# Performance work log

Hardware: AMD Instinct MI355X
Metric: run time of the kernel (lower is better)

Reference implementation:

```python
import jax, jax.numpy as jnp
import numpy as np

POOL = 7
IMG_H, IMG_W = 1024, 1024
CANONICAL = 224.0  # canonical box size used in the FPN level assignment


def _crop_and_resize(fm, boxes, ph, pw):
    """TF-style crop_and_resize (extrapolation_value=0).

    fm: [C, H, W] feature map; boxes: [N, 4] normalized (y1, x1, y2, x2).
    Returns [N, C, ph, pw] bilinearly sampled crops.
    """
    C, H, W = fm.shape
    y1, x1, y2, x2 = boxes[:, 0], boxes[:, 1], boxes[:, 2], boxes[:, 3]
    ty = jnp.arange(ph, dtype=boxes.dtype) / (ph - 1)  # [ph] in [0,1]
    tx = jnp.arange(pw, dtype=boxes.dtype) / (pw - 1)
    ys = (y1[:, None] + (y2 - y1)[:, None] * ty) * (H - 1)  # [N, ph] image coords
    xs = (x1[:, None] + (x2 - x1)[:, None] * tx) * (W - 1)  # [N, pw]
    yy = jnp.broadcast_to(ys[:, :, None], (ys.shape[0], ph, pw))  # [N, ph, pw]
    xx = jnp.broadcast_to(xs[:, None, :], (xs.shape[0], ph, pw))
    y0f = jnp.floor(yy)
    x0f = jnp.floor(xx)
    wy = yy - y0f
    wx = xx - x0f
    y0 = jnp.clip(y0f.astype(jnp.int32), 0, H - 1)
    y1i = jnp.clip(y0 + 1, 0, H - 1)
    x0 = jnp.clip(x0f.astype(jnp.int32), 0, W - 1)
    x1i = jnp.clip(x0 + 1, 0, W - 1)

    def g(yi, xi):
        return fm[:, yi, xi]  # [C, N, ph, pw]

    val = (g(y0, x0) * ((1 - wy) * (1 - wx))[None]
           + g(y0, x1i) * ((1 - wy) * wx)[None]
           + g(y1i, x0) * (wy * (1 - wx))[None]
           + g(y1i, x1i) * (wy * wx)[None])
    # extrapolation_value = 0 for samples outside the feature map
    inb = (yy >= 0) & (yy <= H - 1) & (xx >= 0) & (xx <= W - 1)
    val = jnp.where(inb[None], val, 0.0)
    return jnp.transpose(val, (1, 0, 2, 3))  # [N, C, ph, pw]


def setup_inputs() -> dict:
    key = jax.random.key(0)
    k1, k2, k3, k4, k5, k6, k7, k8 = jax.random.split(key, 8)
    N = 1000
    y1 = jax.random.uniform(k1, (N, 1)) * 0.7
    x1 = jax.random.uniform(k2, (N, 1)) * 0.7
    hh = jax.random.uniform(k3, (N, 1)) * 0.28 + 0.02
    ww = jax.random.uniform(k4, (N, 1)) * 0.28 + 0.02
    boxes = jnp.concatenate([y1, x1, y1 + hh, x1 + ww], axis=1)[None]  # [1,N,4]
    C = 256
    p2 = jax.random.normal(k5, (1, C, 256, 256), dtype=jnp.float32)
    p3 = jax.random.normal(k6, (1, C, 128, 128), dtype=jnp.float32)
    p4 = jax.random.normal(k7, (1, C, 64, 64), dtype=jnp.float32)
    p5 = jax.random.normal(k8, (1, C, 32, 32), dtype=jnp.float32)
    return {"boxes": boxes, "p2": p2, "p3": p3, "p4": p4, "p5": p5}


def reference(boxes, p2, p3, p4, p5):
    boxes = boxes[0]  # squeeze batch, [N,4]
    fms = [p2[0], p3[0], p4[0], p5[0]]  # each [C,H,W]
    y1, x1, y2, x2 = boxes[:, 0:1], boxes[:, 1:2], boxes[:, 2:3], boxes[:, 3:4]
    h = y2 - y1
    w = x2 - x1
    image_area = jnp.asarray(float(IMG_H * IMG_W), dtype=boxes.dtype)
    roi_level = 4 + jnp.log2(jnp.sqrt(h * w) / (CANONICAL / jnp.sqrt(image_area)))
    roi_level = jnp.clip(jnp.round(roi_level), 2, 5).astype(jnp.int32)[:, 0]  # [N]
    # Boxes are detached before cropping in the original (level_boxes.detach()).
    crop_boxes = jax.lax.stop_gradient(boxes)
    out = jnp.zeros((boxes.shape[0], fms[0].shape[0], POOL, POOL), dtype=boxes.dtype)
    for i, level in enumerate(range(2, 6)):
        crop = _crop_and_resize(fms[i], crop_boxes, POOL, POOL)
        sel = (roi_level == level)[:, None, None, None]
        out = out + jnp.where(sel, crop, 0.0)
    return out  # [N, C, POOL, POOL], original box order (sort restores order)
```

## Files before the change

kernel.cpp:

```cpp
#include <hip/hip_runtime.h>

#define POOL 7
#define NCH 256
#define OUT_PER_BOX (NCH * POOL * POOL)
#define PARTS 7
#define PART_SZ (OUT_PER_BOX / PARTS)
#define ITERS (PART_SZ / 256)

__global__ __launch_bounds__(256) void roi_align_kernel(
    const float* __restrict__ boxes,
    const float* __restrict__ p2,
    const float* __restrict__ p3,
    const float* __restrict__ p4,
    const float* __restrict__ p5,
    float* __restrict__ out,
    int nbox)
{
    const int n    = blockIdx.x % nbox;
    const int part = blockIdx.x / nbox;
    const int tid  = threadIdx.x;

    __shared__ int   s_y0[POOL], s_y1[POOL], s_xb[POOL], s_xcl[POOL];
    __shared__ float s_wy[POOL], s_wx[POOL], s_vy[POOL], s_vx[POOL];

    const float by1 = boxes[n * 4 + 0];
    const float bx1 = boxes[n * 4 + 1];
    const float by2 = boxes[n * 4 + 2];
    const float bx2 = boxes[n * 4 + 3];
    const float h = by2 - by1;
    const float w = bx2 - bx1;

    const float lvlf = 4.0f + log2f(sqrtf(h * w) / 0.21875f);
    int lvl = (int)rintf(lvlf);
    lvl = lvl < 2 ? 2 : (lvl > 5 ? 5 : lvl);

    const float* fm;
    int H;
    switch (lvl) {
        case 2:  fm = p2; H = 256; break;
        case 3:  fm = p3; H = 128; break;
        case 4:  fm = p4; H = 64;  break;
        default: fm = p5; H = 32;  break;
    }
    const float Hm1 = (float)(H - 1);

    if (tid < POOL) {
        const float t = (float)tid * (1.0f / 6.0f);

        const float yy  = (by1 + h * t) * Hm1;
        const float y0f = floorf(yy);
        int y0 = (int)y0f;
        y0 = min(H - 1, max(0, y0));
        s_y0[tid] = y0;
        s_y1[tid] = min(H - 1, y0 + 1);
        s_wy[tid] = yy - y0f;
        s_vy[tid] = (yy >= 0.0f && yy <= Hm1) ? 1.0f : 0.0f;

        const float xx  = (bx1 + w * t) * Hm1;
        const float x0f = floorf(xx);
        int x0 = (int)x0f;
        x0 = min(H - 1, max(0, x0));
        s_xb[tid]  = min(x0, H - 2);
        s_xcl[tid] = (x0 == H - 1) ? 1 : 0;
        s_wx[tid]  = xx - x0f;
        s_vx[tid]  = (xx >= 0.0f && xx <= Hm1) ? 1.0f : 0.0f;
    }
    __syncthreads();

    const size_t out_base = (size_t)n * OUT_PER_BOX + (size_t)part * PART_SZ;
    const int idx0 = part * PART_SZ + tid;
    const int HW = H * H;

    float2 q0[ITERS], q1[ITERS];
    #pragma unroll
    for (int i = 0; i < ITERS; ++i) {
        const int idx = idx0 + i * 256;
        const int c  = idx / 49;
        const int r  = idx - c * 49;
        const int py = r / 7;
        const int px = r - py * 7;

        const float* fmc = fm + (size_t)c * HW;
        const int xb = s_xb[px];
        q0[i] = *(const float2*)(fmc + s_y0[py] * H + xb);
        q1[i] = *(const float2*)(fmc + s_y1[py] * H + xb);
    }

    #pragma unroll
    for (int i = 0; i < ITERS; ++i) {
        const int idx = idx0 + i * 256;
        const int c  = idx / 49;
        const int r  = idx - c * 49;
        const int py = r / 7;
        const int px = r - py * 7;

        const float wy = s_wy[py], wx = s_wx[px];
        const int   cl = s_xcl[px];

        const float v00 = cl ? q0[i].y : q0[i].x;
        const float v01 = q0[i].y;
        const float v10 = cl ? q1[i].y : q1[i].x;
        const float v11 = q1[i].y;

        const float r0 = v00 + wx * (v01 - v00);
        const float r1 = v10 + wx * (v11 - v10);
        float val = (r0 + wy * (r1 - r0)) * s_vy[py] * s_vx[px];

        out[out_base + (size_t)(i * 256 + tid)] = val;
    }
}

extern "C" void kernel_launch(void* const* d_in, const int* in_sizes, int n_in,
                              void* d_out, int out_size, void* d_ws, size_t ws_size,
                              hipStream_t stream) {
    const float* boxes = (const float*)d_in[0];
    const float* p2    = (const float*)d_in[1];
    const float* p3    = (const float*)d_in[2];
    const float* p4    = (const float*)d_in[3];
    const float* p5    = (const float*)d_in[4];
    float* out         = (float*)d_out;

    const int nbox = in_sizes[0] / 4;
    roi_align_kernel<<<nbox * PARTS, 256, 0, stream>>>(boxes, p2, p3, p4, p5, out, nbox);
}
```

Before: 155.0 us.

## Sort boxes by level and Morton order and map contiguous chunks per XCD

Adds a single-block bitonic sort that orders boxes by pyramid level and then by the Morton code of their centres, writing a permutation into the workspace. The main kernel now remaps block indices so that each of the 8 XCDs handles a contiguous run of sorted boxes, with all 7 parts of a box landing on the same XCD. The aim is better L2 reuse of feature-map rows, since spatially nearby boxes share samples and stay within one XCD's cache. The cost is an extra kernel launch with a serial sort, and output writes become scattered in box order.

New measurement: 184.8 us. +19.2%, slower.

```diff
diff --git a/kernel.cpp b/kernel.cpp
--- a/kernel.cpp
+++ b/kernel.cpp
@@ -6,6 +6,66 @@
 #define PARTS 7
 #define PART_SZ (OUT_PER_BOX / PARTS)
 #define ITERS (PART_SZ / 256)
+#define NXCD 8
+
+__device__ __forceinline__ unsigned part1by1(unsigned x) {
+    x &= 0x0000FFFFu;
+    x = (x | (x << 8)) & 0x00FF00FFu;
+    x = (x | (x << 4)) & 0x0F0F0F0Fu;
+    x = (x | (x << 2)) & 0x33333333u;
+    x = (x | (x << 1)) & 0x55555555u;
+    return x;
+}
+
+__global__ __launch_bounds__(1024) void sort_boxes_kernel(
+    const float* __restrict__ boxes, int* __restrict__ perm, int nbox)
+{
+    __shared__ unsigned s_key[1024];
+    const int i = threadIdx.x;
+
+    unsigned key = 0xFFFFFFFFu;
+    if (i < nbox) {
+        const float y1 = boxes[i * 4 + 0];
+        const float x1 = boxes[i * 4 + 1];
+        const float y2 = boxes[i * 4 + 2];
+        const float x2 = boxes[i * 4 + 3];
+        const float h = y2 - y1;
+        const float w = x2 - x1;
+        const float lvlf = 4.0f + log2f(sqrtf(h * w) * (1.0f / 0.21875f));
+        int lvl = (int)rintf(lvlf);
+        lvl = lvl < 2 ? 2 : (lvl > 5 ? 5 : lvl);
+
+        const float cy = 0.5f * (y1 + y2);
+        const float cx = 0.5f * (x1 + x2);
+        unsigned qy = (unsigned)fminf(511.0f, fmaxf(0.0f, cy * 512.0f));
+        unsigned qx = (unsigned)fminf(511.0f, fmaxf(0.0f, cx * 512.0f));
+        const unsigned morton = (part1by1(qy) << 1) | part1by1(qx);
+
+        key = ((unsigned)(lvl - 2) << 28) | (morton << 10) | (unsigned)i;
+    }
+    s_key[i] = key;
+    __syncthreads();
+
+    for (int k = 2; k <= 1024; k <<= 1) {
+        for (int j = k >> 1; j > 0; j >>= 1) {
+            const int p = i ^ j;
+            if (p > i) {
+                const unsigned a = s_key[i];
+                const unsigned b = s_key[p];
+                const bool up = ((i & k) == 0);
+                if ((a > b) == up) { s_key[i] = b; s_key[p] = a; }
+            }
+            __syncthreads();
+        }
+    }
+
+    if (i < nbox) perm[i] = (int)(s_key[i] & 1023u);
+}
+
+__global__ void identity_perm_kernel(int* __restrict__ perm, int nbox) {
+    const int i = blockIdx.x * blockDim.x + threadIdx.x;
+    if (i < nbox) perm[i] = i;
+}
 
 __global__ __launch_bounds__(256) void roi_align_kernel(
     const float* __restrict__ boxes,
@@ -14,11 +74,17 @@
     const float* __restrict__ p4,
     const float* __restrict__ p5,
     float* __restrict__ out,
-    int nbox)
+    const int* __restrict__ perm,
+    int nbox, int cpx)
 {
-    const int n    = blockIdx.x % nbox;
-    const int part = blockIdx.x / nbox;
-    const int tid  = threadIdx.x;
+    const int c    = blockIdx.x & (NXCD - 1);
+    const int k    = blockIdx.x >> 3;
+    const int l    = k / PARTS;
+    const int part = k - l * PARTS;
+    const int s    = c * cpx + l;
+    if (s >= nbox) return;
+    const int n = perm[s];
+    const int tid = threadIdx.x;
 
     __shared__ int   s_y0[POOL], s_y1[POOL], s_xb[POOL], s_xcl[POOL];
     __shared__ float s_wy[POOL], s_wx[POOL], s_vy[POOL], s_vx[POOL];
@@ -75,12 +141,12 @@
     #pragma unroll
     for (int i = 0; i < ITERS; ++i) {
         const int idx = idx0 + i * 256;
-        const int c  = idx / 49;
-        const int r  = idx - c * 49;
-        const int py = r / 7;
-        const int px = r - py * 7;
-
-        const float* fmc = fm + (size_t)c * HW;
+        const int cch = idx / 49;
+        const int r   = idx - cch * 49;
+        const int py  = r / 7;
+        const int px  = r - py * 7;
+
+        const float* fmc = fm + (size_t)cch * HW;
         const int xb = s_xb[px];
         q0[i] = *(const float2*)(fmc + s_y0[py] * H + xb);
         q1[i] = *(const float2*)(fmc + s_y1[py] * H + xb);
@@ -89,10 +155,10 @@
     #pragma unroll
     for (int i = 0; i < ITERS; ++i) {
         const int idx = idx0 + i * 256;
-        const int c  = idx / 49;
-        const int r  = idx - c * 49;
-        const int py = r / 7;
-        const int px = r - py * 7;
+        const int cch = idx / 49;
+        const int r   = idx - cch * 49;
+        const int py  = r / 7;
+        const int px  = r - py * 7;
 
         const float wy = s_wy[py], wx = s_wx[px];
         const int   cl = s_xcl[px];
@@ -119,7 +185,17 @@
     const float* p4    = (const float*)d_in[3];
     const float* p5    = (const float*)d_in[4];
     float* out         = (float*)d_out;
+    int*   perm        = (int*)d_ws;
 
     const int nbox = in_sizes[0] / 4;
-    roi_align_kernel<<<nbox * PARTS, 256, 0, stream>>>(boxes, p2, p3, p4, p5, out, nbox);
-}
+    const int cpx  = (nbox + NXCD - 1) / NXCD;
+
+    if (nbox <= 1024) {
+        sort_boxes_kernel<<<1, 1024, 0, stream>>>(boxes, perm, nbox);
+    } else {
+        identity_perm_kernel<<<(nbox + 255) / 256, 256, 0, stream>>>(perm, nbox);
+    }
+
+    roi_align_kernel<<<NXCD * cpx * PARTS, 256, 0, stream>>>(
+        boxes, p2, p3, p4, p5, out, perm, nbox, cpx);
+}
```

## Precompute sorted box params and process box groups per block with software pipelining

Applied to the files above, without the earlier changes.

A prep kernel computes each box's sampling parameters once and counting-sorts boxes by FPN level and spatial quadrant, writing them to workspace. The main kernel then has each block handle a slice of channels for a group of 8 spatially-near, same-level boxes, reading params from shared memory and double-buffering gathers so one box's loads overlap the previous box's interpolation. The goal is better cache locality for feature-map gathers, less redundant per-block setup, and more memory-level parallelism. The cost is an extra kernel launch, and outputs are now written in sorted order, scattered across boxes. A fallback to the old kernel is kept for when workspace is too small.

Measured after the change: 165.8 us. 6.9% more time.

```diff
diff --git a/kernel.cpp b/kernel.cpp
--- a/kernel.cpp
+++ b/kernel.cpp
@@ -3,18 +3,212 @@
 #define POOL 7
 #define NCH 256
 #define OUT_PER_BOX (NCH * POOL * POOL)
-#define PARTS 7
-#define PART_SZ (OUT_PER_BOX / PARTS)
-#define ITERS (PART_SZ / 256)
+#define NSLICE 28
+#define SLICE_SZ (OUT_PER_BOX / NSLICE)
+#define G 8
+#define NBINS 64
+#define PWORDS 64
+
+
+__device__ __forceinline__ void box_params(
+    const float* __restrict__ boxes, int i, int* __restrict__ P, int* lvl_out)
+{
+    const float by1 = boxes[i * 4 + 0];
+    const float bx1 = boxes[i * 4 + 1];
+    const float by2 = boxes[i * 4 + 2];
+    const float bx2 = boxes[i * 4 + 3];
+    const float h = by2 - by1;
+    const float w = bx2 - bx1;
+    const float lvlf = 4.0f + log2f(sqrtf(h * w) / 0.21875f);
+    int lvl = (int)rintf(lvlf);
+    lvl = lvl < 2 ? 2 : (lvl > 5 ? 5 : lvl);
+    const int H = 256 >> (lvl - 2);
+    const float Hm1 = (float)(H - 1);
+
+    #pragma unroll
+    for (int t = 0; t < POOL; ++t) {
+        const float tt = (float)t * (1.0f / 6.0f);
+
+        const float yy  = (by1 + h * tt) * Hm1;
+        const float y0f = floorf(yy);
+        int y0 = (int)y0f;
+        y0 = min(H - 1, max(0, y0));
+        P[t]      = y0 * H;
+        P[7 + t]  = min(H - 1, y0 + 1) * H;
+        P[28 + t] = __float_as_int(yy - y0f);
+        P[42 + t] = __float_as_int((yy >= 0.0f && yy <= Hm1) ? 1.0f : 0.0f);
+
+        const float xx  = (bx1 + w * tt) * Hm1;
+        const float x0f = floorf(xx);
+        int x0 = (int)x0f;
+        x0 = min(H - 1, max(0, x0));
+        P[14 + t] = min(x0, H - 2);
+        P[21 + t] = (x0 == H - 1) ? 1 : 0;
+        P[35 + t] = __float_as_int(xx - x0f);
+        P[49 + t] = __float_as_int((xx >= 0.0f && xx <= Hm1) ? 1.0f : 0.0f);
+    }
+    P[56] = lvl - 2;
+    P[57] = H;
+    P[58] = H * H;
+    P[59] = i;
+    *lvl_out = lvl;
+}
+
+__global__ __launch_bounds__(1024) void prep_kernel(
+    const float* __restrict__ boxes, int* __restrict__ params, int nbox)
+{
+    __shared__ int s_cnt[NBINS], s_off[NBINS];
+    const int i = threadIdx.x;
+    if (i < NBINS) s_cnt[i] = 0;
+    __syncthreads();
+
+    int bin = -1;
+    if (i < nbox) {
+        const float y1 = boxes[i * 4 + 0];
+        const float x1 = boxes[i * 4 + 1];
+        const float y2 = boxes[i * 4 + 2];
+        const float x2 = boxes[i * 4 + 3];
+        const float h = y2 - y1;
+        const float w = x2 - x1;
+        const float lvlf = 4.0f + log2f(sqrtf(h * w) * (1.0f / 0.21875f));
+        int lvl = (int)rintf(lvlf);
+        lvl = lvl < 2 ? 2 : (lvl > 5 ? 5 : lvl);
+        const float cy = 0.5f * (y1 + y2);
+        const float cx = 0.5f * (x1 + x2);
+        int qy = (int)(cy * 4.0f); qy = qy < 0 ? 0 : (qy > 3 ? 3 : qy);
+        int qx = (int)(cx * 4.0f); qx = qx < 0 ? 0 : (qx > 3 ? 3 : qx);
+        bin = ((lvl - 2) << 4) | (qy << 2) | qx;
+        atomicAdd(&s_cnt[bin], 1);
+    }
+    __syncthreads();
+    if (i == 0) {
+        int acc = 0;
+        for (int b = 0; b < NBINS; ++b) { s_off[b] = acc; acc += s_cnt[b]; }
+    }
+    __syncthreads();
+    if (i < nbox) {
+        const int pos = atomicAdd(&s_off[bin], 1);
+        int dummy;
+        box_params(boxes, i, params + pos * PWORDS, &dummy);
+    }
+}
+
+__global__ void prep_flat_kernel(
+    const float* __restrict__ boxes, int* __restrict__ params, int nbox)
+{
+    const int i = blockIdx.x * blockDim.x + threadIdx.x;
+    if (i >= nbox) return;
+    int dummy;
+    box_params(boxes, i, params + i * PWORDS, &dummy);
+}
+
+#define ISSUE(kk, Q00, Q01, Q10, Q11) do {                                   \
+    const int* P = sp[(kk)];                                                 \
+    const int lv = __builtin_amdgcn_readfirstlane(P[56]);                    \
+    const int HW = __builtin_amdgcn_readfirstlane(P[58]);                    \
+    const float* fm = lv == 0 ? p2 : lv == 1 ? p3 : lv == 2 ? p4 : p5;       \
+    { const int a = c0 * HW + P[14 + px0];                                   \
+      Q00 = *(const float2*)(fm + a + P[py0]);                               \
+      Q01 = *(const float2*)(fm + a + P[7 + py0]); }                         \
+    if (has1) {                                                              \
+      const int a = c1 * HW + P[14 + px1];                                   \
+      Q10 = *(const float2*)(fm + a + P[py1]);                               \
+      Q11 = *(const float2*)(fm + a + P[7 + py1]); }                         \
+} while (0)
+
+#define FINISH(kk, Q00, Q01, Q10, Q11) do {                                  \
+    const int* P = sp[(kk)];                                                 \
+    const int n = __builtin_amdgcn_readfirstlane(P[59]);                     \
+    const size_t ob = (size_t)n * OUT_PER_BOX + s * SLICE_SZ + tid;          \
+    {                                                                        \
+        const float wy = __int_as_float(P[28 + py0]);                        \
+        const float wx = __int_as_float(P[35 + px0]);                        \
+        const float vv = __int_as_float(P[42 + py0]) *                       \
+                         __int_as_float(P[49 + px0]);                        \
+        const int   cl = P[21 + px0];                                        \
+        const float v00 = cl ? Q00.y : Q00.x;                                \
+        const float v01 = Q00.y;                                             \
+        const float v10 = cl ? Q01.y : Q01.x;                                \
+        const float v11 = Q01.y;                                             \
+        const float r0v = v00 + wx * (v01 - v00);                            \
+        const float r1v = v10 + wx * (v11 - v10);                            \
+        out[ob] = (r0v + wy * (r1v - r0v)) * vv;                             \
+    }                                                                        \
+    if (has1) {                                                              \
+        const float wy = __int_as_float(P[28 + py1]);                        \
+        const float wx = __int_as_float(P[35 + px1]);                        \
+        const float vv = __int_as_float(P[42 + py1]) *                       \
+                         __int_as_float(P[49 + px1]);                        \
+        const int   cl = P[21 + px1];                                        \
+        const float v00 = cl ? Q10.y : Q10.x;                                \
+        const float v01 = Q10.y;                                             \
+        const float v10 = cl ? Q11.y : Q11.x;                                \
+        const float v11 = Q11.y;                                             \
+        const float r0v = v00 + wx * (v01 - v00);                            \
+        const float r1v = v10 + wx * (v11 - v10);                            \
+        out[ob + 256] = (r0v + wy * (r1v - r0v)) * vv;                       \
+    }                                                                        \
+} while (0)
 
 __global__ __launch_bounds__(256) void roi_align_kernel(
-    const float* __restrict__ boxes,
     const float* __restrict__ p2,
     const float* __restrict__ p3,
     const float* __restrict__ p4,
     const float* __restrict__ p5,
     float* __restrict__ out,
+    const int* __restrict__ params,
     int nbox)
+{
+    const int s   = blockIdx.x % NSLICE;
+    const int g   = blockIdx.x / NSLICE;
+    const int tid = threadIdx.x;
+    const int base = g * G;
+    const int cnt  = min(G, nbox - base);
+
+    __shared__ int sp[G][PWORDS];
+    {
+        const int total = cnt * PWORDS;
+        for (int j = tid; j < G * PWORDS; j += 256)
+            sp[0][j] = (j < total) ? params[base * PWORDS + j] : 0;
+    }
+    __syncthreads();
+
+    const int idx0 = s * SLICE_SZ + tid;
+    const int c0  = idx0 / 49;
+    const int r0  = idx0 - c0 * 49;
+    const int py0 = r0 / 7;
+    const int px0 = r0 - py0 * 7;
+    const bool has1 = (tid < SLICE_SZ - 256);
+    const int idx1 = idx0 + 256;
+    const int c1  = idx1 / 49;
+    const int r1  = idx1 - c1 * 49;
+    const int py1 = r1 / 7;
+    const int px1 = r1 - py1 * 7;
+
+    float2 A00 = {0,0}, A01 = {0,0}, A10 = {0,0}, A11 = {0,0};
+    float2 B00 = {0,0}, B01 = {0,0}, B10 = {0,0}, B11 = {0,0};
+
+    ISSUE(0, A00, A01, A10, A11);
+    #pragma unroll
+    for (int k = 0; k < G; k += 2) {
+        if (k >= cnt) break;
+        if (k + 1 < cnt) ISSUE(k + 1, B00, B01, B10, B11);
+        FINISH(k, A00, A01, A10, A11);
+        if (k + 1 >= cnt) break;
+        if (k + 2 < cnt) ISSUE(k + 2, A00, A01, A10, A11);
+        FINISH(k + 1, B00, B01, B10, B11);
+    }
+}
+
+#define PARTS 7
+#define PART_SZ (OUT_PER_BOX / PARTS)
+#define ITERS (PART_SZ / 256)
+
+__global__ __launch_bounds__(256) void roi_align_flat_kernel(
+    const float* __restrict__ boxes,
+    const float* __restrict__ p2, const float* __restrict__ p3,
+    const float* __restrict__ p4, const float* __restrict__ p5,
+    float* __restrict__ out, int nbox)
 {
     const int n    = blockIdx.x % nbox;
     const int part = blockIdx.x / nbox;
@@ -29,7 +223,6 @@
     const float bx2 = boxes[n * 4 + 3];
     const float h = by2 - by1;
     const float w = bx2 - bx1;
-
     const float lvlf = 4.0f + log2f(sqrtf(h * w) / 0.21875f);
     int lvl = (int)rintf(lvlf);
     lvl = lvl < 2 ? 2 : (lvl > 5 ? 5 : lvl);
@@ -46,7 +239,6 @@
 
     if (tid < POOL) {
         const float t = (float)tid * (1.0f / 6.0f);
-
         const float yy  = (by1 + h * t) * Hm1;
         const float y0f = floorf(yy);
         int y0 = (int)y0f;
@@ -55,7 +247,6 @@
         s_y1[tid] = min(H - 1, y0 + 1);
         s_wy[tid] = yy - y0f;
         s_vy[tid] = (yy >= 0.0f && yy <= Hm1) ? 1.0f : 0.0f;
-
         const float xx  = (bx1 + w * t) * Hm1;
         const float x0f = floorf(xx);
         int x0 = (int)x0f;
@@ -79,13 +270,11 @@
         const int r  = idx - c * 49;
         const int py = r / 7;
         const int px = r - py * 7;
-
         const float* fmc = fm + (size_t)c * HW;
         const int xb = s_xb[px];
         q0[i] = *(const float2*)(fmc + s_y0[py] * H + xb);
         q1[i] = *(const float2*)(fmc + s_y1[py] * H + xb);
     }
-
     #pragma unroll
     for (int i = 0; i < ITERS; ++i) {
         const int idx = idx0 + i * 256;
@@ -93,20 +282,15 @@
         const int r  = idx - c * 49;
         const int py = r / 7;
         const int px = r - py * 7;
-
         const float wy = s_wy[py], wx = s_wx[px];
         const int   cl = s_xcl[px];
-
         const float v00 = cl ? q0[i].y : q0[i].x;
         const float v01 = q0[i].y;
         const float v10 = cl ? q1[i].y : q1[i].x;
         const float v11 = q1[i].y;
-
         const float r0 = v00 + wx * (v01 - v00);
         const float r1 = v10 + wx * (v11 - v10);
-        float val = (r0 + wy * (r1 - r0)) * s_vy[py] * s_vx[px];
-
-        out[out_base + (size_t)(i * 256 + tid)] = val;
+        out[out_base + (size_t)(i * 256 + tid)] = (r0 + wy * (r1 - r0)) * s_vy[py] * s_vx[px];
     }
 }
 
@@ -121,5 +305,22 @@
     float* out         = (float*)d_out;
 
     const int nbox = in_sizes[0] / 4;
-    roi_align_kernel<<<nbox * PARTS, 256, 0, stream>>>(boxes, p2, p3, p4, p5, out, nbox);
-}
+    const size_t need = (size_t)nbox * PWORDS * sizeof(int);
+
+    if (ws_size < need) {
+        roi_align_flat_kernel<<<nbox * PARTS, 256, 0, stream>>>(
+            boxes, p2, p3, p4, p5, out, nbox);
+        return;
+    }
+
+    int* params = (int*)d_ws;
+    if (nbox <= 1024) {
+        prep_kernel<<<1, 1024, 0, stream>>>(boxes, params, nbox);
+    } else {
+        prep_flat_kernel<<<(nbox + 255) / 256, 256, 0, stream>>>(boxes, params, nbox);
+    }
+
+    const int ngroups = (nbox + G - 1) / G;
+    roi_align_kernel<<<ngroups * NSLICE, 256, 0, stream>>>(
+        p2, p3, p4, p5, out, params, nbox);
+}
```

## Bin ROIs by level and spatial tile, stage shared feature regions in LDS

Applied to the files above, without the earlier changes.

Adds a prep pass that precomputes per-box sampling parameters and buckets level 3-5 boxes into spatial bins with atomically tracked bounding regions. A main kernel then loads each bin's feature-map window for a few channels into LDS once and serves every box in the bin from it, so overlapping boxes reuse the same data. Level-2 boxes keep the direct-gather path through a compacted list. This costs two extra launches, atomics, a serial per-bin loop over boxes, and writes scattered across boxes, with fallback to global reads when the region exceeds LDS.

New measurement: 201.0 us. +29.7%, slower.

```diff
diff --git a/kernel.cpp b/kernel.cpp
--- a/kernel.cpp
+++ b/kernel.cpp
@@ -6,22 +6,47 @@
 #define PARTS 7
 #define PART_SZ (OUT_PER_BOX / PARTS)
 #define ITERS (PART_SZ / 256)
-
-__global__ __launch_bounds__(256) void roi_align_kernel(
-    const float* __restrict__ boxes,
-    const float* __restrict__ p2,
-    const float* __restrict__ p3,
-    const float* __restrict__ p4,
-    const float* __restrict__ p5,
-    float* __restrict__ out,
-    int nbox)
+#define PWORDS 64
+
+#define QGRID 4
+#define NBIN_L (QGRID * QGRID)
+#define NLVL_BINNED 3
+#define NBINS (NBIN_L * NLVL_BINNED)
+#define L2BIN NBINS
+#define NLISTS (NBINS + 1)
+
+#define C3 2
+#define C4 4
+#define C5 4
+#define NCHUNK3 (NCH / C3)
+#define NCHUNK4 (NCH / C4)
+#define NCHUNK5 (NCH / C5)
+#define NBLK3 (NBIN_L * NCHUNK3)
+#define NBLK4 (NBIN_L * NCHUNK4)
+#define NBLK5 (NBIN_L * NCHUNK5)
+#define NBLK_BINNED (NBLK3 + NBLK4 + NBLK5)
+
+#define REGION_FLOATS 12288
+
+
+__global__ void init_kernel(int* __restrict__ meta) {
+    const int i = threadIdx.x;
+    if (i < NLISTS) {
+        meta[i * 8 + 0] = 0;
+        meta[i * 8 + 1] = 0x7fffffff;
+        meta[i * 8 + 2] = -1;
+        meta[i * 8 + 3] = 0x7fffffff;
+        meta[i * 8 + 4] = -1;
+    }
+}
+
+__global__ __launch_bounds__(256) void prep_kernel(
+    const float* __restrict__ boxes, int* __restrict__ params,
+    int* __restrict__ meta, int* __restrict__ lists, int nbox)
 {
-    const int n    = blockIdx.x % nbox;
-    const int part = blockIdx.x / nbox;
-    const int tid  = threadIdx.x;
-
-    __shared__ int   s_y0[POOL], s_y1[POOL], s_xb[POOL], s_xcl[POOL];
-    __shared__ float s_wy[POOL], s_wx[POOL], s_vy[POOL], s_vx[POOL];
+    const int n = blockIdx.x * 4 + (threadIdx.x >> 6);
+    const int j = threadIdx.x & 63;
+    if (n >= nbox) return;
 
     const float by1 = boxes[n * 4 + 0];
     const float bx1 = boxes[n * 4 + 1];
@@ -29,7 +54,246 @@
     const float bx2 = boxes[n * 4 + 3];
     const float h = by2 - by1;
     const float w = bx2 - bx1;
-
+    const float lvlf = 4.0f + log2f(sqrtf(h * w) / 0.21875f);
+    int lvl = (int)rintf(lvlf);
+    lvl = lvl < 2 ? 2 : (lvl > 5 ? 5 : lvl);
+    const int H = 256 >> (lvl - 2);
+    const float Hm1 = (float)(H - 1);
+
+    const int t = j % 7;
+    const float tt = (float)t * (1.0f / 6.0f);
+
+    const float yy  = (by1 + h * tt) * Hm1;
+    const float y0f = floorf(yy);
+    int y0 = (int)y0f; y0 = min(H - 1, max(0, y0));
+    const int y1c = min(H - 1, y0 + 1);
+
+    const float xx  = (bx1 + w * tt) * Hm1;
+    const float x0f = floorf(xx);
+    int x0 = (int)x0f; x0 = min(H - 1, max(0, x0));
+    const int xb  = min(x0, H - 2);
+    const int xcl = (x0 == H - 1) ? 1 : 0;
+
+    int val;
+    switch (j / 7) {
+        case 0: val = y0;   break;
+        case 1: val = y1c;  break;
+        case 2: val = xb;   break;
+        case 3: val = xcl;  break;
+        case 4: val = __float_as_int(yy - y0f); break;
+        case 5: val = __float_as_int(xx - x0f); break;
+        case 6: val = __float_as_int((yy >= 0.0f && yy <= Hm1) ? 1.0f : 0.0f); break;
+        case 7: val = __float_as_int((xx >= 0.0f && xx <= Hm1) ? 1.0f : 0.0f); break;
+        default: {
+            const int r = j - 56;
+            val = (r == 0) ? (lvl - 2) : (r == 1) ? H : (r == 2) ? H * H
+                : (r == 3) ? n : 0;
+        }
+    }
+    params[n * PWORDS + j] = val;
+
+    if (j == 0) {
+        if (lvl == 2) {
+            const int slot = atomicAdd(&meta[L2BIN * 8 + 0], 1);
+            lists[L2BIN * nbox + slot] = n;
+        } else {
+            const float cy = 0.5f * (by1 + by2);
+            const float cx = 0.5f * (bx1 + bx2);
+            int qy = (int)(cy * 4.0f); qy = qy < 0 ? 0 : (qy > 3 ? 3 : qy);
+            int qx = (int)(cx * 4.0f); qx = qx < 0 ? 0 : (qx > 3 ? 3 : qx);
+            const int bin = (lvl - 3) * NBIN_L + qy * QGRID + qx;
+            const int slot = atomicAdd(&meta[bin * 8 + 0], 1);
+            lists[bin * nbox + slot] = n;
+            const float yy6 = (by1 + h) * Hm1;
+            int y06 = (int)floorf(yy6); y06 = min(H - 1, max(0, y06));
+            const int y16 = min(H - 1, y06 + 1);
+            const float xx6 = (bx1 + w) * Hm1;
+            int x06 = (int)floorf(xx6); x06 = min(H - 1, max(0, x06));
+            const int xb6 = min(x06, H - 2);
+            atomicMin(&meta[bin * 8 + 1], y0);
+            atomicMax(&meta[bin * 8 + 2], y16);
+            atomicMin(&meta[bin * 8 + 3], xb);
+            atomicMax(&meta[bin * 8 + 4], xb6 + 1);
+        }
+    }
+}
+
+__global__ __launch_bounds__(256) void main_kernel(
+    const float* __restrict__ p2,
+    const float* __restrict__ p3,
+    const float* __restrict__ p4,
+    const float* __restrict__ p5,
+    float* __restrict__ out,
+    const int* __restrict__ params,
+    const int* __restrict__ meta,
+    const int* __restrict__ lists,
+    int nbox)
+{
+    __shared__ float region[REGION_FLOATS];
+    __shared__ int sPm[2 * PWORDS];
+
+    const int bid = blockIdx.x;
+    const int tid = threadIdx.x;
+
+    if (bid >= NBLK_BINNED) {
+        const int bid2 = bid - NBLK_BINNED;
+        const int rank = bid2 / PARTS;
+        const int part = bid2 - rank * PARTS;
+        if (rank >= meta[L2BIN * 8 + 0]) return;
+        const int n = lists[L2BIN * nbox + rank];
+        if (tid < PWORDS) sPm[tid] = params[n * PWORDS + tid];
+        __syncthreads();
+        const float* fm = p2;
+        const int H = 256, HW = 65536;
+
+        const size_t out_base = (size_t)n * OUT_PER_BOX + (size_t)part * PART_SZ;
+        const int idx0 = part * PART_SZ + tid;
+
+        float2 q0[ITERS], q1[ITERS];
+        #pragma unroll
+        for (int i = 0; i < ITERS; ++i) {
+            const int idx = idx0 + i * 256;
+            const int c  = idx / 49;
+            const int r  = idx - c * 49;
+            const int py = r / 7;
+            const int px = r - py * 7;
+            const float* fmc = fm + (size_t)c * HW;
+            const int xb = sPm[14 + px];
+            q0[i] = *(const float2*)(fmc + sPm[py] * H + xb);
+            q1[i] = *(const float2*)(fmc + sPm[7 + py] * H + xb);
+        }
+        #pragma unroll
+        for (int i = 0; i < ITERS; ++i) {
+            const int idx = idx0 + i * 256;
+            const int c  = idx / 49;
+            const int r  = idx - c * 49;
+            const int py = r / 7;
+            const int px = r - py * 7;
+            const float wy = __int_as_float(sPm[28 + py]);
+            const float wx = __int_as_float(sPm[35 + px]);
+            const int   cl = sPm[21 + px];
+            const float v00 = cl ? q0[i].y : q0[i].x;
+            const float v01 = q0[i].y;
+            const float v10 = cl ? q1[i].y : q1[i].x;
+            const float v11 = q1[i].y;
+            const float r0 = v00 + wx * (v01 - v00);
+            const float r1 = v10 + wx * (v11 - v10);
+            out[out_base + (size_t)(i * 256 + tid)] =
+                (r0 + wy * (r1 - r0)) * __int_as_float(sPm[42 + py])
+                                      * __int_as_float(sPm[49 + px]);
+        }
+        return;
+    }
+
+    int b = bid;
+    int lvlm, bin, c0, C, BPP;
+    if (b < NBLK3)              { lvlm = 0; bin = b / NCHUNK3; c0 = (b % NCHUNK3) * C3; C = C3; BPP = 2; }
+    else if (b < NBLK3 + NBLK4) { b -= NBLK3; lvlm = 1; bin = b / NCHUNK4; c0 = (b % NCHUNK4) * C4; C = C4; BPP = 1; }
+    else                        { b -= NBLK3 + NBLK4; lvlm = 2; bin = b / NCHUNK5; c0 = (b % NCHUNK5) * C5; C = C5; BPP = 1; }
+
+    const int gbin = lvlm * NBIN_L + bin;
+    const int cnt  = meta[gbin * 8 + 0];
+    if (cnt == 0) return;
+
+    const int H  = 128 >> lvlm;
+    const int HW = H * H;
+    const float* fm = (lvlm == 0) ? p3 : (lvlm == 1) ? p4 : p5;
+
+    const int by0 = meta[gbin * 8 + 1];
+    const int by1 = meta[gbin * 8 + 2];
+    const int bx0 = meta[gbin * 8 + 3] & ~3;
+    const int bx1 = meta[gbin * 8 + 4];
+    const int R   = by1 - by0 + 1;
+    const int n4  = (bx1 - bx0 + 4) >> 2;
+    const int W   = n4 * 4;
+    const bool use_lds = (C * R * W) <= REGION_FLOATS;
+
+    if (use_lds) {
+        const int RW4 = R * n4;
+        const int tot = C * RW4;
+        for (int q = tid; q < tot; q += 256) {
+            const int c    = q / RW4;
+            const int rem2 = q - c * RW4;
+            const int r    = rem2 / n4;
+            const int w4   = rem2 - r * n4;
+            const float4 v = *(const float4*)(fm + (size_t)(c0 + c) * HW
+                                              + (by0 + r) * H + bx0 + w4 * 4);
+            *(float4*)&region[(c * R + r) * W + w4 * 4] = v;
+        }
+    }
+
+    const int npb  = C * 49;
+    const int act  = BPP * npb;
+    const int bsel = tid / npb;
+    const int rem  = tid - bsel * npb;
+    const int cl   = rem / 49;
+    const int pos  = rem - cl * 49;
+    const int py   = pos / 7;
+    const int px   = pos - py * 7;
+    const int obase = (c0 + cl) * 49 + pos;
+
+    for (int k = 0; k < cnt; k += BPP) {
+        __syncthreads();
+        if (tid < BPP * PWORDS) {
+            const int bb = tid >> 6;
+            const int kk2 = k + bb;
+            if (kk2 < cnt)
+                sPm[tid] = params[lists[gbin * nbox + kk2] * PWORDS + (tid & 63)];
+        }
+        __syncthreads();
+        const int kk = k + bsel;
+        if (tid < act && kk < cnt) {
+            const int* P = sPm + bsel * PWORDS;
+            const int r0 = P[py]     - by0;
+            const int r1 = P[7 + py] - by0;
+            const int xo = P[14 + px] - bx0;
+            const int clx = P[21 + px];
+            float v00, v01, v10, v11;
+            if (use_lds) {
+                const float* base = &region[cl * R * W];
+                v00 = base[r0 * W + xo + clx];
+                v01 = base[r0 * W + xo + 1];
+                v10 = base[r1 * W + xo + clx];
+                v11 = base[r1 * W + xo + 1];
+            } else {
+                const float* basep = fm + (size_t)(c0 + cl) * HW;
+                const int xa = P[14 + px];
+                v00 = basep[P[py] * H + xa + clx];
+                v01 = basep[P[py] * H + xa + 1];
+                v10 = basep[P[7 + py] * H + xa + clx];
+                v11 = basep[P[7 + py] * H + xa + 1];
+            }
+            const float wy = __int_as_float(P[28 + py]);
+            const float wx = __int_as_float(P[35 + px]);
+            const float a0 = v00 + wx * (v01 - v00);
+            const float a1 = v10 + wx * (v11 - v10);
+            const float val = (a0 + wy * (a1 - a0))
+                              * __int_as_float(P[42 + py])
+                              * __int_as_float(P[49 + px]);
+            out[(size_t)P[59] * OUT_PER_BOX + obase] = val;
+        }
+    }
+}
+
+__global__ __launch_bounds__(256) void roi_align_flat_kernel(
+    const float* __restrict__ boxes,
+    const float* __restrict__ p2, const float* __restrict__ p3,
+    const float* __restrict__ p4, const float* __restrict__ p5,
+    float* __restrict__ out, int nbox)
+{
+    const int n    = blockIdx.x % nbox;
+    const int part = blockIdx.x / nbox;
+    const int tid  = threadIdx.x;
+
+    __shared__ int   s_y0[POOL], s_y1[POOL], s_xb[POOL], s_xcl[POOL];
+    __shared__ float s_wy[POOL], s_wx[POOL], s_vy[POOL], s_vx[POOL];
+
+    const float by1 = boxes[n * 4 + 0];
+    const float bx1 = boxes[n * 4 + 1];
+    const float by2 = boxes[n * 4 + 2];
+    const float bx2 = boxes[n * 4 + 3];
+    const float h = by2 - by1;
+    const float w = bx2 - bx1;
     const float lvlf = 4.0f + log2f(sqrtf(h * w) / 0.21875f);
     int lvl = (int)rintf(lvlf);
     lvl = lvl < 2 ? 2 : (lvl > 5 ? 5 : lvl);
@@ -46,7 +310,6 @@
 
     if (tid < POOL) {
         const float t = (float)tid * (1.0f / 6.0f);
-
         const float yy  = (by1 + h * t) * Hm1;
         const float y0f = floorf(yy);
         int y0 = (int)y0f;
@@ -55,7 +318,6 @@
         s_y1[tid] = min(H - 1, y0 + 1);
         s_wy[tid] = yy - y0f;
         s_vy[tid] = (yy >= 0.0f && yy <= Hm1) ? 1.0f : 0.0f;
-
         const float xx  = (bx1 + w * t) * Hm1;
         const float x0f = floorf(xx);
         int x0 = (int)x0f;
@@ -79,13 +341,11 @@
         const int r  = idx - c * 49;
         const int py = r / 7;
         const int px = r - py * 7;
-
         const float* fmc = fm + (size_t)c * HW;
         const int xb = s_xb[px];
         q0[i] = *(const float2*)(fmc + s_y0[py] * H + xb);
         q1[i] = *(const float2*)(fmc + s_y1[py] * H + xb);
     }
-
     #pragma unroll
     for (int i = 0; i < ITERS; ++i) {
         const int idx = idx0 + i * 256;
@@ -93,20 +353,16 @@
         const int r  = idx - c * 49;
         const int py = r / 7;
         const int px = r - py * 7;
-
         const float wy = s_wy[py], wx = s_wx[px];
         const int   cl = s_xcl[px];
-
         const float v00 = cl ? q0[i].y : q0[i].x;
         const float v01 = q0[i].y;
         const float v10 = cl ? q1[i].y : q1[i].x;
         const float v11 = q1[i].y;
-
         const float r0 = v00 + wx * (v01 - v00);
         const float r1 = v10 + wx * (v11 - v10);
-        float val = (r0 + wy * (r1 - r0)) * s_vy[py] * s_vx[px];
-
-        out[out_base + (size_t)(i * 256 + tid)] = val;
+        out[out_base + (size_t)(i * 256 + tid)] =
+            (r0 + wy * (r1 - r0)) * s_vy[py] * s_vx[px];
     }
 }
 
@@ -121,5 +377,23 @@
     float* out         = (float*)d_out;
 
     const int nbox = in_sizes[0] / 4;
-    roi_align_kernel<<<nbox * PARTS, 256, 0, stream>>>(boxes, p2, p3, p4, p5, out, nbox);
-}
+    const size_t params_b = (size_t)nbox * PWORDS * sizeof(int);
+    const size_t meta_b   = (size_t)NLISTS * 8 * sizeof(int);
+    const size_t lists_b  = (size_t)NLISTS * nbox * sizeof(int);
+    const size_t need     = params_b + meta_b + lists_b;
+
+    if (ws_size < need) {
+        roi_align_flat_kernel<<<nbox * PARTS, 256, 0, stream>>>(
+            boxes, p2, p3, p4, p5, out, nbox);
+        return;
+    }
+
+    int* params = (int*)d_ws;
+    int* meta   = (int*)((char*)d_ws + params_b);
+    int* lists  = (int*)((char*)d_ws + params_b + meta_b);
+
+    init_kernel<<<1, 64, 0, stream>>>(meta);
+    prep_kernel<<<(nbox + 3) / 4, 256, 0, stream>>>(boxes, params, meta, lists, nbox);
+    main_kernel<<<NBLK_BINNED + nbox * PARTS, 256, 0, stream>>>(
+        p2, p3, p4, p5, out, params, meta, lists, nbox);
+}
```
